# Kernel optimization log

Measured on AMD Instinct MI355X. Metric: run time of the kernel, lower is better.

The kernel has to match this reference:

```python
import jax, jax.numpy as jnp
import numpy as np

B, IN, H = 4096, 1024, 2048

def setup_inputs() -> dict:
    key = jax.random.key(0)
    ks = jax.random.split(key, 7)
    sk = (1.0 / H) ** 0.5
    return {
        "x": jax.random.normal(ks[0], (B, IN), dtype=jnp.float32),
        "prev_h": jax.random.normal(ks[1], (B, H), dtype=jnp.float32),
        "prev_c": jax.random.normal(ks[2], (B, H), dtype=jnp.float32),
        "W_i": jax.random.uniform(ks[3], (H, H + IN), dtype=jnp.float32, minval=-sk, maxval=sk),
        "W_f": jax.random.uniform(ks[4], (H, H + IN), dtype=jnp.float32, minval=-sk, maxval=sk),
        "W_o": jax.random.uniform(ks[5], (H, H + IN), dtype=jnp.float32, minval=-sk, maxval=sk),
        "W_c": jax.random.uniform(ks[6], (H, H + IN), dtype=jnp.float32, minval=-sk, maxval=sk),
    }

def reference(x, prev_h, prev_c, W_i, W_f, W_o, W_c):
    # concat (h, x) along features: [B, H+IN]
    hx = jnp.concatenate([prev_h, x], axis=1)
    # stack 4 gate weights -> single GEMM: [B, H+IN] @ [H+IN, 4H]
    W = jnp.concatenate([W_i, W_f, W_o, W_c], axis=0)  # [4H, H+IN]
    gates = hx @ W.T  # [B, 4H]
    gi, gf, go, gc = jnp.split(gates, 4, axis=1)
    i = jax.nn.sigmoid(gi)
    f = jax.nn.sigmoid(gf)
    o = jax.nn.sigmoid(go)
    c_tilde = jnp.tanh(gc)
    next_c = f * prev_c + i * c_tilde
    next_h = o * jnp.tanh(next_c)
    return next_h, next_c
```

## Files before the change

kernel.cpp:

```cpp
#include <hip/hip_runtime.h>
#include <hip/hip_bf16.h>


#define BATCH 4096
#define INW   1024
#define HID   2048
#define GK    3072
#define GN    8192

typedef __attribute__((ext_vector_type(8))) short short8;
typedef __attribute__((ext_vector_type(4))) float floatx4;

__device__ __forceinline__ unsigned short f2bf(float f) {
    union { float f; unsigned u; } v; v.f = f;
    unsigned r = v.u + 0x7FFFu + ((v.u >> 16) & 1u);
    return (unsigned short)(r >> 16);
}
__device__ __forceinline__ float bf2f(unsigned short u) {
    union { unsigned u; float f; } v; v.u = ((unsigned)u) << 16;
    return v.f;
}
__device__ __forceinline__ float sigf(float x) {
    return 1.0f / (1.0f + __expf(-x));
}
__device__ __forceinline__ float tanhfast(float x) {
    float t = __expf(fminf(fmaxf(2.0f * x, -30.0f), 30.0f));
    return (t - 1.0f) / (t + 1.0f);
}

__global__ __launch_bounds__(256) void pack_all(const float4* __restrict__ ph,
                                                const float4* __restrict__ x,
                                                const float4* __restrict__ Wi,
                                                const float4* __restrict__ Wf,
                                                const float4* __restrict__ Wo,
                                                const float4* __restrict__ Wc,
                                                unsigned short* __restrict__ hx,
                                                unsigned short* __restrict__ Wb) {
    long i = (long)blockIdx.x * 256 + threadIdx.x;
    const float4* src;
    unsigned short* dst;
    if (i < 1048576L) {
        int r  = (int)(i >> 8);
        int c8 = (int)(i & 255);
        src = ph + 2 * i;
        dst = hx + (size_t)r * GK + (size_t)c8 * 8;
    } else if (i < 1572864L) {
        long j = i - 1048576L;
        int r  = (int)(j >> 7);
        int c8 = (int)(j & 127);
        src = x + 2 * j;
        dst = hx + (size_t)r * GK + HID + (size_t)c8 * 8;
    } else {
        long j = i - 1572864L;
        const float4* Wg;
        int g;
        if (j < 786432L)            { Wg = Wi; g = 0; }
        else if (j < 1572864L)      { Wg = Wf; g = 1; j -= 786432L; }
        else if (j < 2359296L)      { Wg = Wo; g = 2; j -= 1572864L; }
        else                        { Wg = Wc; g = 3; j -= 2359296L; }
        src = Wg + 2 * j;
        dst = Wb + (size_t)g * HID * GK + (size_t)j * 8;
    }
    float4 v0 = src[0];
    float4 v1 = src[1];
    unsigned short o[8];
    o[0] = f2bf(v0.x); o[1] = f2bf(v0.y); o[2] = f2bf(v0.z); o[3] = f2bf(v0.w);
    o[4] = f2bf(v1.x); o[5] = f2bf(v1.y); o[6] = f2bf(v1.z); o[7] = f2bf(v1.w);
    *(short8*)dst = *(const short8*)o;
}

__device__ __forceinline__ void gld16(const unsigned short* g, unsigned short* l) {
    __builtin_amdgcn_global_load_lds((const __attribute__((address_space(1))) unsigned int*)g,
                                     (__attribute__((address_space(3))) unsigned int*)l,
                                     16, 0, 0);
}

__global__ __launch_bounds__(256) void gemm_bt(const unsigned short* __restrict__ A,
                                               const unsigned short* __restrict__ Bt,
                                               unsigned short* __restrict__ C) {
    __shared__ unsigned short lA[128 * 32];
    __shared__ unsigned short lB[128 * 32];
    const int tid  = threadIdx.x;
    const int wave = tid >> 6;
    const int lane = tid & 63;
    const long row0 = (long)blockIdx.x * 128;
    const long col0 = (long)blockIdx.y * 128;

    const int sr = tid >> 2;
    const int sk = (tid & 3) << 3;
    const unsigned short* gA0 = A  + (row0 + sr)      * GK + sk;
    const unsigned short* gA1 = A  + (row0 + 64 + sr) * GK + sk;
    const unsigned short* gB0 = Bt + (col0 + sr)      * GK + sk;
    const unsigned short* gB1 = Bt + (col0 + 64 + sr) * GK + sk;
    unsigned short* lA0 = &lA[wave * 512];
    unsigned short* lA1 = &lA[2048 + wave * 512];
    unsigned short* lB0 = &lB[wave * 512];
    unsigned short* lB1 = &lB[2048 + wave * 512];

    floatx4 acc[4][4];
    #pragma unroll
    for (int mi = 0; mi < 4; mi++)
        #pragma unroll
        for (int ni = 0; ni < 4; ni++)
            acc[mi][ni] = (floatx4)(0.0f);

    const int mBase = (wave >> 1) << 6;
    const int nBase = (wave & 1) << 6;
    const int fr = lane & 15;
    const int kq = (lane >> 4) << 3;

    for (int k0 = 0; k0 < GK; k0 += 32) {
        __syncthreads();
        gld16(gA0 + k0, lA0);
        gld16(gA1 + k0, lA1);
        gld16(gB0 + k0, lB0);
        gld16(gB1 + k0, lB1);
        __syncthreads();

        short8 af[4], bfv[4];
        #pragma unroll
        for (int mi = 0; mi < 4; mi++)
            af[mi] = *(const short8*)&lA[(mBase + mi * 16 + fr) * 32 + kq];
        #pragma unroll
        for (int ni = 0; ni < 4; ni++)
            bfv[ni] = *(const short8*)&lB[(nBase + ni * 16 + fr) * 32 + kq];
        #pragma unroll
        for (int mi = 0; mi < 4; mi++)
            #pragma unroll
            for (int ni = 0; ni < 4; ni++)
                acc[mi][ni] = __builtin_amdgcn_mfma_f32_16x16x32_bf16(af[mi], bfv[ni], acc[mi][ni], 0, 0, 0);
    }

    const int cr = (lane >> 4) << 2;
    const int cc = lane & 15;
    #pragma unroll
    for (int mi = 0; mi < 4; mi++) {
        #pragma unroll
        for (int ni = 0; ni < 4; ni++) {
            long base = (row0 + mBase + mi * 16 + cr) * (long)GN + col0 + nBase + ni * 16 + cc;
            #pragma unroll
            for (int r = 0; r < 4; r++)
                C[base + (long)r * GN] = f2bf(acc[mi][ni][r]);
        }
    }
}

__global__ __launch_bounds__(256) void lstm_ep(const unsigned short* __restrict__ gates,
                                               const float* __restrict__ prev_c,
                                               float* __restrict__ out) {
    const int i = blockIdx.x * 256 + threadIdx.x;
    const int b = i >> 9;
    const int h = (i & 511) << 2;
    const size_t gb = (size_t)b * GN + h;
    ushort4 gi = *(const ushort4*)&gates[gb];
    ushort4 gf = *(const ushort4*)&gates[gb + HID];
    ushort4 go = *(const ushort4*)&gates[gb + 2 * HID];
    ushort4 gc = *(const ushort4*)&gates[gb + 3 * HID];
    const size_t ob = (size_t)b * HID + h;
    float4 c4 = *(const float4*)&prev_c[ob];

    unsigned short giv[4] = {gi.x, gi.y, gi.z, gi.w};
    unsigned short gfv[4] = {gf.x, gf.y, gf.z, gf.w};
    unsigned short gov[4] = {go.x, go.y, go.z, go.w};
    unsigned short gcv[4] = {gc.x, gc.y, gc.z, gc.w};
    float cv[4] = {c4.x, c4.y, c4.z, c4.w};
    float nh[4], nc[4];
    #pragma unroll
    for (int j = 0; j < 4; j++) {
        float vi = sigf(bf2f(giv[j]));
        float vf = sigf(bf2f(gfv[j]));
        float vo = sigf(bf2f(gov[j]));
        float vc = tanhfast(bf2f(gcv[j]));
        float ncf = vf * cv[j] + vi * vc;
        float nhf = vo * tanhfast(ncf);
        nc[j] = ncf;
        nh[j] = nhf;
    }
    float4 vh = {nh[0], nh[1], nh[2], nh[3]};
    float4 vc4 = {nc[0], nc[1], nc[2], nc[3]};
    *(float4*)&out[ob] = vh;
    *(float4*)&out[(size_t)BATCH * HID + ob] = vc4;
}

extern "C" void kernel_launch(void* const* d_in, const int* in_sizes, int n_in,
                              void* d_out, int out_size, void* d_ws, size_t ws_size,
                              hipStream_t stream) {
    const float* x   = (const float*)d_in[0];
    const float* ph  = (const float*)d_in[1];
    const float* pc  = (const float*)d_in[2];
    const float* Wi  = (const float*)d_in[3];
    const float* Wf  = (const float*)d_in[4];
    const float* Wo  = (const float*)d_in[5];
    const float* Wc  = (const float*)d_in[6];

    unsigned short* hx    = (unsigned short*)d_ws;
    unsigned short* Wb    = hx + (size_t)BATCH * GK;
    unsigned short* gates = Wb + (size_t)GN * GK;
    float* out = (float*)d_out;

    pack_all<<<18432, 256, 0, stream>>>((const float4*)ph, (const float4*)x,
                                        (const float4*)Wi, (const float4*)Wf,
                                        (const float4*)Wo, (const float4*)Wc,
                                        hx, Wb);

    gemm_bt<<<dim3(BATCH / 128, GN / 128), 256, 0, stream>>>(hx, Wb, gates);

    lstm_ep<<<(BATCH * HID / 4) / 256, 256, 0, stream>>>(gates, pc, out);
}
```

Measured before the change: 456.8 us.

## Double GEMM K-tile to 64 with XOR-rotated LDS layout to avoid bank conflicts

Each main-loop iteration of the bf16 GEMM now stages a 64-wide K slice instead of 32, which halves the number of barrier pairs and global-load rounds. LDS rows are stored with a per-row rotated chunk index (swizzle) so the fragment reads for the MFMAs spread across banks. LDS use doubles to 32 KB per block, which may lower occupancy, and loads are still not overlapped with compute.

```diff
diff --git a/kernel.cpp b/kernel.cpp
--- a/kernel.cpp
+++ b/kernel.cpp
@@ -78,24 +78,26 @@
 __global__ __launch_bounds__(256) void gemm_bt(const unsigned short* __restrict__ A,
                                                const unsigned short* __restrict__ Bt,
                                                unsigned short* __restrict__ C) {
-    __shared__ unsigned short lA[128 * 32];
-    __shared__ unsigned short lB[128 * 32];
+    __shared__ unsigned short lA[128 * 64];
+    __shared__ unsigned short lB[128 * 64];
     const int tid  = threadIdx.x;
     const int wave = tid >> 6;
     const int lane = tid & 63;
     const long row0 = (long)blockIdx.x * 128;
     const long col0 = (long)blockIdx.y * 128;
 
-    const int sr = tid >> 2;
-    const int sk = (tid & 3) << 3;
-    const unsigned short* gA0 = A  + (row0 + sr)      * GK + sk;
-    const unsigned short* gA1 = A  + (row0 + 64 + sr) * GK + sk;
-    const unsigned short* gB0 = Bt + (col0 + sr)      * GK + sk;
-    const unsigned short* gB1 = Bt + (col0 + 64 + sr) * GK + sk;
-    unsigned short* lA0 = &lA[wave * 512];
-    unsigned short* lA1 = &lA[2048 + wave * 512];
-    unsigned short* lB0 = &lB[wave * 512];
-    unsigned short* lB1 = &lB[2048 + wave * 512];
+    const int r_loc = tid >> 3;
+    const int c0    = ((tid & 7) - r_loc) & 7;
+
+    const unsigned short* gA[4];
+    const unsigned short* gB[4];
+    #pragma unroll
+    for (int j = 0; j < 4; j++) {
+        gA[j] = A  + (row0 + j * 32 + r_loc) * GK + c0 * 8;
+        gB[j] = Bt + (col0 + j * 32 + r_loc) * GK + c0 * 8;
+    }
+    unsigned short* lAs = &lA[tid * 8];
+    unsigned short* lBs = &lB[tid * 8];
 
     floatx4 acc[4][4];
     #pragma unroll
@@ -107,28 +109,36 @@
     const int mBase = (wave >> 1) << 6;
     const int nBase = (wave & 1) << 6;
     const int fr = lane & 15;
-    const int kq = (lane >> 4) << 3;
-
-    for (int k0 = 0; k0 < GK; k0 += 32) {
+    const int cq = lane >> 4;
+
+    for (int k0 = 0; k0 < GK; k0 += 64) {
         __syncthreads();
-        gld16(gA0 + k0, lA0);
-        gld16(gA1 + k0, lA1);
-        gld16(gB0 + k0, lB0);
-        gld16(gB1 + k0, lB1);
+        #pragma unroll
+        for (int j = 0; j < 4; j++) gld16(gA[j] + k0, lAs + j * 2048);
+        #pragma unroll
+        for (int j = 0; j < 4; j++) gld16(gB[j] + k0, lBs + j * 2048);
         __syncthreads();
 
-        short8 af[4], bfv[4];
-        #pragma unroll
-        for (int mi = 0; mi < 4; mi++)
-            af[mi] = *(const short8*)&lA[(mBase + mi * 16 + fr) * 32 + kq];
-        #pragma unroll
-        for (int ni = 0; ni < 4; ni++)
-            bfv[ni] = *(const short8*)&lB[(nBase + ni * 16 + fr) * 32 + kq];
-        #pragma unroll
-        for (int mi = 0; mi < 4; mi++)
-            #pragma unroll
-            for (int ni = 0; ni < 4; ni++)
-                acc[mi][ni] = __builtin_amdgcn_mfma_f32_16x16x32_bf16(af[mi], bfv[ni], acc[mi][ni], 0, 0, 0);
+        #pragma unroll
+        for (int ks = 0; ks < 2; ks++) {
+            const int ci = ks * 4 + cq;
+            short8 af[4], bfv[4];
+            #pragma unroll
+            for (int mi = 0; mi < 4; mi++) {
+                int R = mBase + mi * 16 + fr;
+                af[mi] = *(const short8*)&lA[R * 64 + (((ci + R) & 7) << 3)];
+            }
+            #pragma unroll
+            for (int ni = 0; ni < 4; ni++) {
+                int R = nBase + ni * 16 + fr;
+                bfv[ni] = *(const short8*)&lB[R * 64 + (((ci + R) & 7) << 3)];
+            }
+            #pragma unroll
+            for (int mi = 0; mi < 4; mi++)
+                #pragma unroll
+                for (int ni = 0; ni < 4; ni++)
+                    acc[mi][ni] = __builtin_amdgcn_mfma_f32_16x16x32_bf16(af[mi], bfv[ni], acc[mi][ni], 0, 0, 0);
+        }
     }
 
     const int cr = (lane >> 4) << 2;
```

Measured after the change: 418.9 us. -8.3%, faster.
